# Kernel optimization log

Hardware: AMD Instinct MI355X
Metric: run time of the kernel (lower is better)

## Reference

```python
import jax, jax.numpy as jnp
import numpy as np
from jax import lax

SOBEL_X = jnp.array([[-1., 0., 1.], [-2., 0., 2.], [-1., 0., 1.]], jnp.float32)
SCHARR_X = jnp.array([[-3., 0., 3.], [-10., 0., 10.], [-3., 0., 3.]], jnp.float32)

# year routing map baked in (configure()): 2019->sobel(0), 2020->scharr(1), default learnable(2)

def _dwconv(x, k2d):
    """Depthwise 3x3 conv with the same 2D kernel per channel, padding=1."""
    C = x.shape[1]
    kern = jnp.broadcast_to(k2d, (C, 1, 3, 3))
    return lax.conv_general_dilated(
        x, kern, window_strides=(1, 1), padding='SAME',
        dimension_numbers=('NCHW', 'OIHW', 'NCHW'), feature_group_count=C)


def _edge_mag(x, kx, ky, eps):
    gx = _dwconv(x, kx)
    gy = _dwconv(x, ky)
    return jnp.sqrt(gx * gx + gy * gy + eps)


def setup_inputs() -> dict:
    key = jax.random.key(0)
    k1, k2 = jax.random.split(key)
    x = jax.random.normal(k1, (32, 9, 256, 256), jnp.float32)
    year = 2018 + jax.random.randint(k2, (32,), 0, 4)  # years 2018..2021
    alpha = jnp.asarray(0.5, jnp.float32)
    scale = jnp.ones((1,), jnp.float32) * 0.1
    return {"x": x, "alpha": alpha, "scale": scale, "year": year}


def reference(x, alpha, scale, year):
    B = x.shape[0]
    # fixed operators
    sobel_out = _edge_mag(x, SOBEL_X, SOBEL_X.T, 1e-8)
    scharr_out = _edge_mag(x, SCHARR_X, SCHARR_X.T, 1e-8)
    # learnable operator: sigmoid-mixed kernel, normalized by max abs
    a = jax.nn.sigmoid(alpha)
    kx = a * SOBEL_X + (1.0 - a) * SCHARR_X
    kx = kx / jnp.max(jnp.abs(kx))
    ky = kx.T  # sobel_y = sobel_x.T and scharr_y = scharr_x.T, mix commutes with transpose
    learnable_out = _edge_mag(x, kx, ky, 1e-6) * jax.nn.sigmoid(scale)
    # per-sample routing: 2019 -> sobel, 2020 -> scharr, else default learnable
    op_idx = jnp.where(year == 2019, 0, jnp.where(year == 2020, 1, 2))
    stacked = jnp.stack([sobel_out, scharr_out, learnable_out])  # [3,B,C,H,W]
    mixed = stacked[op_idx, jnp.arange(B)]
    return mixed
```

## Files before the change

kernel.cpp:

```cpp
#include <hip/hip_runtime.h>
#include <math.h>

#define BATCH 32
#define CHANS 9
#define HH 256
#define WW 256

typedef float f32x4 __attribute__((ext_vector_type(4)));

__global__ __launch_bounds__(256) void edge_router_kernel(
    const float* __restrict__ x,
    const float* __restrict__ alpha_p,
    const float* __restrict__ scale_p,
    const int*   __restrict__ year,
    float* __restrict__ out)
{
    const int tid   = threadIdx.x;
    const int lane  = tid & 63;
    const int gwave = blockIdx.x * 4 + (tid >> 6);
    const int row   = gwave & (HH - 1);
    const int plane = gwave >> 8;
    const int b     = plane / CHANS;
    const int xq    = lane * 4;

    const float* __restrict__ p = x   + (size_t)plane * (HH * WW);
    float*       __restrict__ q = out + (size_t)plane * (HH * WW);

    const int ym = row > 0 ? row - 1 : 0;
    const int yp = row < HH - 1 ? row + 1 : HH - 1;
    f32x4 vm = *reinterpret_cast<const f32x4*>(p + (size_t)ym  * WW + xq);
    f32x4 v0 = *reinterpret_cast<const f32x4*>(p + (size_t)row * WW + xq);
    f32x4 vp = *reinterpret_cast<const f32x4*>(p + (size_t)yp  * WW + xq);
    if (row == 0)      vm = (f32x4)0.f;
    if (row == HH - 1) vp = (f32x4)0.f;

    const int yr = year[b];
    float w0, w1, eps, post;
    if (yr == 2019) {
        w0 = 1.f; w1 = 2.f; eps = 1e-8f; post = 1.f;
    } else if (yr == 2020) {
        w0 = 3.f; w1 = 10.f; eps = 1e-8f; post = 1.f;
    } else {
        const float a = 1.f / (1.f + expf(-alpha_p[0]));
        const float m = 10.f - 8.f * a;
        w0 = (3.f - 2.f * a) / m;
        w1 = 1.f;
        eps = 1e-6f;
        post = 1.f / (1.f + expf(-scale_p[0]));
    }

    auto derive = [&](f32x4 vv, f32x4& d, f32x4& s) {
        float left  = __shfl_up(vv.w, 1);
        if (lane == 0)  left  = 0.f;
        float right = __shfl_down(vv.x, 1);
        if (lane == 63) right = 0.f;
        d.x = vv.y - left;  d.y = vv.z - vv.x;
        d.z = vv.w - vv.y;  d.w = right - vv.z;
        s.x = fmaf(w1, vv.x, w0 * (left + vv.y));
        s.y = fmaf(w1, vv.y, w0 * (vv.x + vv.z));
        s.z = fmaf(w1, vv.z, w0 * (vv.y + vv.w));
        s.w = fmaf(w1, vv.w, w0 * (vv.z + right));
    };

    f32x4 dm, sm, d0, s0v, dp, sp;
    derive(vm, dm, sm);
    derive(v0, d0, s0v);
    derive(vp, dp, sp);

    f32x4 o;
    {
        float gx = fmaf(w1, d0.x, w0 * (dm.x + dp.x));
        float gy = sp.x - sm.x;
        o.x = sqrtf(fmaf(gx, gx, fmaf(gy, gy, eps))) * post;
    }
    {
        float gx = fmaf(w1, d0.y, w0 * (dm.y + dp.y));
        float gy = sp.y - sm.y;
        o.y = sqrtf(fmaf(gx, gx, fmaf(gy, gy, eps))) * post;
    }
    {
        float gx = fmaf(w1, d0.z, w0 * (dm.z + dp.z));
        float gy = sp.z - sm.z;
        o.z = sqrtf(fmaf(gx, gx, fmaf(gy, gy, eps))) * post;
    }
    {
        float gx = fmaf(w1, d0.w, w0 * (dm.w + dp.w));
        float gy = sp.w - sm.w;
        o.w = sqrtf(fmaf(gx, gx, fmaf(gy, gy, eps))) * post;
    }

    *reinterpret_cast<f32x4*>(q + (size_t)row * WW + xq) = o;
}

extern "C" void kernel_launch(void* const* d_in, const int* in_sizes, int n_in,
                              void* d_out, int out_size, void* d_ws, size_t ws_size,
                              hipStream_t stream) {
    const float* x     = (const float*)d_in[0];
    const float* alpha = (const float*)d_in[1];
    const float* scale = (const float*)d_in[2];
    const int*   year  = (const int*)  d_in[3];
    float* out = (float*)d_out;

    const int rows   = BATCH * CHANS * HH;
    const int blocks = rows / 4;
    edge_router_kernel<<<blocks, 256, 0, stream>>>(x, alpha, scale, year, out);
}
```

Before: 133.8 us.

## Process two rows per wave and separate vertical pass before horizontal shuffles

Each wave now computes two adjacent output rows, loading four input rows instead of three per output row, which cuts redundant global reads from 3x to 2x. The separable stencil is reordered so the vertical smoothing and difference are done first, with lane shuffles applied only to the two intermediate vectors per row. This halves the number of waves and blocks, which lowers parallelism and latency hiding on a memory-bound kernel.

```diff
diff --git a/kernel.cpp b/kernel.cpp
--- a/kernel.cpp
+++ b/kernel.cpp
@@ -18,21 +18,24 @@
     const int tid   = threadIdx.x;
     const int lane  = tid & 63;
     const int gwave = blockIdx.x * 4 + (tid >> 6);
-    const int row   = gwave & (HH - 1);
-    const int plane = gwave >> 8;
+    const int pair  = gwave & 127;
+    const int plane = gwave >> 7;
     const int b     = plane / CHANS;
+    const int r0    = pair * 2;
+    const int r1    = r0 + 1;
     const int xq    = lane * 4;
 
     const float* __restrict__ p = x   + (size_t)plane * (HH * WW);
     float*       __restrict__ q = out + (size_t)plane * (HH * WW);
 
-    const int ym = row > 0 ? row - 1 : 0;
-    const int yp = row < HH - 1 ? row + 1 : HH - 1;
-    f32x4 vm = *reinterpret_cast<const f32x4*>(p + (size_t)ym  * WW + xq);
-    f32x4 v0 = *reinterpret_cast<const f32x4*>(p + (size_t)row * WW + xq);
-    f32x4 vp = *reinterpret_cast<const f32x4*>(p + (size_t)yp  * WW + xq);
-    if (row == 0)      vm = (f32x4)0.f;
-    if (row == HH - 1) vp = (f32x4)0.f;
+    const int ym = r0 > 0 ? r0 - 1 : 0;
+    const int yp = r1 < HH - 1 ? r1 + 1 : HH - 1;
+    f32x4 va = *reinterpret_cast<const f32x4*>(p + (size_t)ym * WW + xq);
+    f32x4 vb = *reinterpret_cast<const f32x4*>(p + (size_t)r0 * WW + xq);
+    f32x4 vc = *reinterpret_cast<const f32x4*>(p + (size_t)r1 * WW + xq);
+    f32x4 vd = *reinterpret_cast<const f32x4*>(p + (size_t)yp * WW + xq);
+    if (r0 == 0)      va = (f32x4)0.f;
+    if (r1 == HH - 1) vd = (f32x4)0.f;
 
     const int yr = year[b];
     float w0, w1, eps, post;
@@ -49,47 +52,45 @@
         post = 1.f / (1.f + expf(-scale_p[0]));
     }
 
-    auto derive = [&](f32x4 vv, f32x4& d, f32x4& s) {
-        float left  = __shfl_up(vv.w, 1);
-        if (lane == 0)  left  = 0.f;
-        float right = __shfl_down(vv.x, 1);
-        if (lane == 63) right = 0.f;
-        d.x = vv.y - left;  d.y = vv.z - vv.x;
-        d.z = vv.w - vv.y;  d.w = right - vv.z;
-        s.x = fmaf(w1, vv.x, w0 * (left + vv.y));
-        s.y = fmaf(w1, vv.y, w0 * (vv.x + vv.z));
-        s.z = fmaf(w1, vv.z, w0 * (vv.y + vv.w));
-        s.w = fmaf(w1, vv.w, w0 * (vv.z + right));
+    auto finish_row = [&](f32x4 t, f32x4 u, int y) {
+        float tl = __shfl_up(t.w, 1);
+        float ul = __shfl_up(u.w, 1);
+        if (lane == 0)  { tl = 0.f; ul = 0.f; }
+        float tr = __shfl_down(t.x, 1);
+        float ur = __shfl_down(u.x, 1);
+        if (lane == 63) { tr = 0.f; ur = 0.f; }
+
+        f32x4 gx, gy;
+        gx.x = t.y - tl;   gx.y = t.z - t.x;
+        gx.z = t.w - t.y;  gx.w = tr - t.z;
+        gy.x = fmaf(w1, u.x, w0 * (ul + u.y));
+        gy.y = fmaf(w1, u.y, w0 * (u.x + u.z));
+        gy.z = fmaf(w1, u.z, w0 * (u.y + u.w));
+        gy.w = fmaf(w1, u.w, w0 * (u.z + ur));
+
+        f32x4 o;
+        o.x = sqrtf(fmaf(gx.x, gx.x, fmaf(gy.x, gy.x, eps))) * post;
+        o.y = sqrtf(fmaf(gx.y, gx.y, fmaf(gy.y, gy.y, eps))) * post;
+        o.z = sqrtf(fmaf(gx.z, gx.z, fmaf(gy.z, gy.z, eps))) * post;
+        o.w = sqrtf(fmaf(gx.w, gx.w, fmaf(gy.w, gy.w, eps))) * post;
+
+        *reinterpret_cast<f32x4*>(q + (size_t)y * WW + xq) = o;
     };
 
-    f32x4 dm, sm, d0, s0v, dp, sp;
-    derive(vm, dm, sm);
-    derive(v0, d0, s0v);
-    derive(vp, dp, sp);
+    f32x4 t0, u0, t1, u1;
+    t0.x = fmaf(w1, vb.x, w0 * (va.x + vc.x));
+    t0.y = fmaf(w1, vb.y, w0 * (va.y + vc.y));
+    t0.z = fmaf(w1, vb.z, w0 * (va.z + vc.z));
+    t0.w = fmaf(w1, vb.w, w0 * (va.w + vc.w));
+    u0 = vc - va;
+    t1.x = fmaf(w1, vc.x, w0 * (vb.x + vd.x));
+    t1.y = fmaf(w1, vc.y, w0 * (vb.y + vd.y));
+    t1.z = fmaf(w1, vc.z, w0 * (vb.z + vd.z));
+    t1.w = fmaf(w1, vc.w, w0 * (vb.w + vd.w));
+    u1 = vd - vb;
 
-    f32x4 o;
-    {
-        float gx = fmaf(w1, d0.x, w0 * (dm.x + dp.x));
-        float gy = sp.x - sm.x;
-        o.x = sqrtf(fmaf(gx, gx, fmaf(gy, gy, eps))) * post;
-    }
-    {
-        float gx = fmaf(w1, d0.y, w0 * (dm.y + dp.y));
-        float gy = sp.y - sm.y;
-        o.y = sqrtf(fmaf(gx, gx, fmaf(gy, gy, eps))) * post;
-    }
-    {
-        float gx = fmaf(w1, d0.z, w0 * (dm.z + dp.z));
-        float gy = sp.z - sm.z;
-        o.z = sqrtf(fmaf(gx, gx, fmaf(gy, gy, eps))) * post;
-    }
-    {
-        float gx = fmaf(w1, d0.w, w0 * (dm.w + dp.w));
-        float gy = sp.w - sm.w;
-        o.w = sqrtf(fmaf(gx, gx, fmaf(gy, gy, eps))) * post;
-    }
-
-    *reinterpret_cast<f32x4*>(q + (size_t)row * WW + xq) = o;
+    finish_row(t0, u0, r0);
+    finish_row(t1, u1, r1);
 }
 
 extern "C" void kernel_launch(void* const* d_in, const int* in_sizes, int n_in,
@@ -101,7 +102,7 @@
     const int*   year  = (const int*)  d_in[3];
     float* out = (float*)d_out;
 
-    const int rows   = BATCH * CHANS * HH;
-    const int blocks = rows / 4;
+    const int pairs  = BATCH * CHANS * (HH / 2);
+    const int blocks = pairs / 4;
     edge_router_kernel<<<blocks, 256, 0, stream>>>(x, alpha, scale, year, out);
 }
```

Result: no change. 132.3 us (-1.1%).
